# Kernel optimization log

Measured on AMD Instinct MI355X. Metric: run time of the kernel, lower is better.

The kernel has to match this reference:

```python
import jax, jax.numpy as jnp
import numpy as np

P_CLASSES = 1024   # num_classes_per_batch
K_SAMP = 4         # num_samples_per_class
MARGIN = 1.0
EPS = 1e-6
EMBED_DIM = 128


def setup_inputs() -> dict:
    key = jax.random.key(0)
    x = jax.random.normal(key, (P_CLASSES * K_SAMP, EMBED_DIM), dtype=jnp.float32)
    return {"x": x}


def reference(x):
    p, k = P_CLASSES, K_SAMP
    n = p * k
    # pairwise distances D[i,j] = sqrt(relu(|xi|^2 - 2 xi.xj + |xj|^2) + eps)
    norms = jnp.sum(x * x, axis=1)
    D = norms[:, None] - 2.0 * (x @ x.T) + norms[None, :]
    D = jnp.sqrt(jax.nn.relu(D) + EPS)  # [n, n]

    # all positive pairs (i<j) within each class, vectorized over classes
    ii, jj = np.triu_indices(k, 1)                      # [m], m = k*(k-1)/2
    c = np.arange(p)
    ri = (c[:, None] * k + ii[None, :]).reshape(-1)     # [P] = [p*m]
    rj = (c[:, None] * k + jj[None, :]).reshape(-1)
    pair_cls = np.repeat(c, len(ii))                    # class of each pair
    col_cls = np.arange(n) // k                         # class of each column
    neg_mask = jnp.asarray(pair_cls[:, None] != col_cls[None, :])  # [P, n]

    # masked logsumexp over negatives from both anchor rows (concat of the
    # two sliced rows in the original code)
    rows = jnp.concatenate([D[ri], D[rj]], axis=1)                 # [P, 2n]
    mask2 = jnp.concatenate([neg_mask, neg_mask], axis=1)
    vals = jnp.where(mask2, MARGIN - rows, -jnp.inf)
    lse = jax.scipy.special.logsumexp(vals, axis=1)                # [P]

    J = lse + D[ri, rj]
    return jnp.mean(jnp.square(jax.nn.relu(J))) / 2.0
```

## Files before the change

kernel.cpp:

```cpp
#include <hip/hip_runtime.h>

#define NROWS 4096
#define DIM 128
#define PCLS 1024
#define NPAIR 6144
#define MARGIN 1.0f
#define EPS 1e-6f
#define LOG2E 1.4426950408889634f
#define NSPLIT 32

typedef __attribute__((ext_vector_type(8))) short bf16x8;
typedef __attribute__((ext_vector_type(4))) float f32x4;

union FragU { uint4 u; bf16x8 v; };

__device__ __forceinline__ unsigned short f2bf(float f) {
    unsigned int b = __float_as_uint(f);
    b = (b + 0x7FFFu + ((b >> 16) & 1u)) >> 16;
    return (unsigned short)b;
}
__device__ __forceinline__ float bf2f(unsigned short u) {
    return __uint_as_float((unsigned int)u << 16);
}

__global__ void prep_kernel(const float* __restrict__ x,
                            unsigned short* __restrict__ xbf,
                            float* __restrict__ norms) {
    int row = blockIdx.x * 4 + (threadIdx.x >> 6);
    int l = threadIdx.x & 63;
    float2 v = *reinterpret_cast<const float2*>(x + row * DIM + 2 * l);
    unsigned int packed = (unsigned int)f2bf(v.x) | ((unsigned int)f2bf(v.y) << 16);
    *reinterpret_cast<unsigned int*>(xbf + row * DIM + 2 * l) = packed;
    float s = v.x * v.x + v.y * v.y;
    #pragma unroll
    for (int m = 1; m < 64; m <<= 1) s += __shfl_xor(s, m, 64);
    if (l == 0) norms[row] = s;
}

__launch_bounds__(512, 4)
__global__ void main_kernel(const unsigned short* __restrict__ xbf,
                            const float* __restrict__ norms,
                            unsigned short* __restrict__ partial,
                            float* __restrict__ posD) {
    __shared__ __align__(16) unsigned short lds[128 * DIM];
    __shared__ float colW[8 * 128];
    const int t = threadIdx.x;
    const int w = t >> 6;
    const int l = t & 63;
    const int lg = l >> 4;
    const int lr = l & 15;

    int u = blockIdx.x;
    int rb = (int)((65.0f - sqrtf(4225.0f - 8.0f * (float)u)) * 0.5f);
    while (rb > 0 && rb * (65 - rb) / 2 > u) --rb;
    while ((rb + 1) * (64 - rb) / 2 <= u) ++rb;
    const int cb = rb + (u - rb * (65 - rb) / 2);
    const bool offd = (cb != rb);

    const int rbase = rb * 128 + w * 16;
    const int cbase = cb * 128;

    FragU afr[4];
    const char* abase = (const char*)xbf + (size_t)(rbase + lr) * 256 + lg * 16;
    #pragma unroll
    for (int s = 0; s < 4; ++s)
        afr[s].u = *reinterpret_cast<const uint4*>(abase + s * 64);

    float njv[8];
    #pragma unroll
    for (int tile = 0; tile < 8; ++tile)
        njv[tile] = norms[cbase + tile * 16 + lr];

    float ni[4];
    #pragma unroll
    for (int rr = 0; rr < 4; ++rr)
        ni[rr] = norms[rbase + lg * 4 + rr] + EPS;

    #pragma unroll
    for (int it = 0; it < 4; ++it) {
        int lin = it * 8192 + t * 16;
        int col = lin >> 8;
        int inner = lin & 255;
        uint4 v = *reinterpret_cast<const uint4*>(
            (const char*)xbf + (size_t)(cbase + col) * 256 + inner);
        *reinterpret_cast<uint4*>(
            (char*)lds + col * 256 + (inner ^ ((col & 7) << 4))) = v;
    }

    __syncthreads();

    float accS[4] = {0.f, 0.f, 0.f, 0.f};
    float colA[8];

    #pragma unroll
    for (int tile = 0; tile < 8; ++tile) {
        const int lcol = tile * 16 + lr;
        const float nj = njv[tile];
        const char* bbase = (const char*)lds + lcol * 256;
        const int xr = (lcol & 7) << 4;
        f32x4 acc = {0.f, 0.f, 0.f, 0.f};
        #pragma unroll
        for (int s = 0; s < 4; ++s) {
            FragU bu;
            int inner = s * 64 + lg * 16;
            bu.u = *reinterpret_cast<const uint4*>(bbase + (inner ^ xr));
            acc = __builtin_amdgcn_mfma_f32_16x16x32_bf16(afr[s].v, bu.v, acc, 0, 0, 0);
        }
        if (offd) {
            float es = 0.f;
            #pragma unroll
            for (int rr = 0; rr < 4; ++rr) {
                float nn = ni[rr] + nj;
                float d2 = fmaf(-2.0f, acc[rr], nn);
                float d = __builtin_amdgcn_sqrtf(fmaxf(d2, EPS));
                float e = __builtin_amdgcn_exp2f(fmaf(d, -LOG2E, LOG2E));
                accS[rr] += e;
                es += e;
            }
            colA[tile] = es;
        } else if (tile != w) {
            #pragma unroll
            for (int rr = 0; rr < 4; ++rr) {
                float nn = ni[rr] + nj;
                float d2 = fmaf(-2.0f, acc[rr], nn);
                float d = __builtin_amdgcn_sqrtf(fmaxf(d2, EPS));
                accS[rr] += __builtin_amdgcn_exp2f(fmaf(d, -LOG2E, LOG2E));
            }
        } else {
            #pragma unroll
            for (int rr = 0; rr < 4; ++rr) {
                int a = lg * 4 + rr;
                int b = lr;
                float nn = ni[rr] + nj;
                float d2 = fmaf(-2.0f, acc[rr], nn);
                float d = __builtin_amdgcn_sqrtf(fmaxf(d2, EPS));
                float e = __builtin_amdgcn_exp2f(fmaf(d, -LOG2E, LOG2E));
                bool same = (a >> 2) == (b >> 2);
                accS[rr] += same ? 0.f : e;
                if (same && a < b) {
                    int i = a & 3, j = b & 3;
                    int idx = i * (7 - i) / 2 + (j - i - 1);
                    int cls = (rbase + a) >> 2;
                    posD[cls * 6 + idx] = d;
                }
            }
        }
    }

    #pragma unroll
    for (int rr = 0; rr < 4; ++rr) {
        #pragma unroll
        for (int m = 1; m < 16; m <<= 1) accS[rr] += __shfl_xor(accS[rr], m, 64);
    }
    if (lr == 0) {
        #pragma unroll
        for (int rr = 0; rr < 4; ++rr)
            partial[cb * NROWS + rbase + lg * 4 + rr] = f2bf(accS[rr]);
    }

    if (offd) {
        #pragma unroll
        for (int tile = 0; tile < 8; ++tile) {
            colA[tile] += __shfl_xor(colA[tile], 16, 64);
            colA[tile] += __shfl_xor(colA[tile], 32, 64);
        }
        if (l < 16) {
            #pragma unroll
            for (int tile = 0; tile < 8; ++tile)
                colW[w * 128 + tile * 16 + l] = colA[tile];
        }
        __syncthreads();
        if (t < 128) {
            float s = 0.f;
            #pragma unroll
            for (int ww = 0; ww < 8; ++ww) s += colW[ww * 128 + t];
            partial[rb * NROWS + cbase + t] = f2bf(s);
        }
    }
}

__global__ void tail_kernel(const unsigned short* __restrict__ partial,
                            const float* __restrict__ posD,
                            float* __restrict__ out) {
    const int c = threadIdx.x;
    float S[4] = {0.f, 0.f, 0.f, 0.f};
    #pragma unroll
    for (int sp = 0; sp < NSPLIT; ++sp) {
        ushort4 v = *reinterpret_cast<const ushort4*>(partial + sp * NROWS + 4 * c);
        S[0] += bf2f(v.x); S[1] += bf2f(v.y); S[2] += bf2f(v.z); S[3] += bf2f(v.w);
    }
    const int II[6] = {0, 0, 0, 1, 1, 2};
    const int JJ[6] = {1, 2, 3, 2, 3, 3};
    float acc = 0.f;
    #pragma unroll
    for (int p = 0; p < 6; ++p) {
        float d = posD[c * 6 + p];
        float J = __logf(S[II[p]] + S[JJ[p]]) + d;
        float r = fmaxf(J, 0.f);
        acc += r * r;
    }
    #pragma unroll
    for (int m = 1; m < 64; m <<= 1) acc += __shfl_xor(acc, m, 64);
    __shared__ float red[16];
    if ((c & 63) == 0) red[c >> 6] = acc;
    __syncthreads();
    if (c < 64) {
        float v = (c < 16) ? red[c] : 0.f;
        #pragma unroll
        for (int m = 1; m < 16; m <<= 1) v += __shfl_xor(v, m, 64);
        if (c == 0) out[0] = v * (1.0f / (2.0f * (float)NPAIR));
    }
}

extern "C" void kernel_launch(void* const* d_in, const int* in_sizes, int n_in,
                              void* d_out, int out_size, void* d_ws, size_t ws_size,
                              hipStream_t stream) {
    const float* x = (const float*)d_in[0];
    char* ws = (char*)d_ws;
    unsigned short* xbf = (unsigned short*)ws;
    float* norms = (float*)(ws + 1048576);
    unsigned short* partial = (unsigned short*)(ws + 1048576 + 16384);
    float* posD = (float*)(ws + 1048576 + 16384 + 262144);
    float* out = (float*)d_out;

    hipLaunchKernelGGL(prep_kernel, dim3(NROWS / 4), dim3(256), 0, stream, x, xbf, norms);
    hipLaunchKernelGGL(main_kernel, dim3(528), dim3(512), 0, stream, xbf, norms, partial, posD);
    hipLaunchKernelGGL(tail_kernel, dim3(1), dim3(1024), 0, stream, partial, posD, out);
}
```

Before: 25.51 us.

## Fuse bf16 conversion and norm computation into main kernel, drop prep kernel

Removes the separate prep kernel that converted x to bf16 and computed row norms. The main kernel now reads fp32 x directly, computes norms for its 256 rows into shared memory, and converts A fragments and B tiles to bf16 on the fly. This saves a kernel launch and the round trip of the bf16 copy through global memory. In exchange each block recomputes norms and conversions, reads twice as many bytes of fp32 input, and adds more ALU work before the first barrier.

```diff
diff --git a/kernel.cpp b/kernel.cpp
--- a/kernel.cpp
+++ b/kernel.cpp
@@ -12,7 +12,7 @@
 typedef __attribute__((ext_vector_type(8))) short bf16x8;
 typedef __attribute__((ext_vector_type(4))) float f32x4;
 
-union FragU { uint4 u; bf16x8 v; };
+union FragU { uint4 u; bf16x8 v; ushort us[8]; };
 
 __device__ __forceinline__ unsigned short f2bf(float f) {
     unsigned int b = __float_as_uint(f);
@@ -23,27 +23,13 @@
     return __uint_as_float((unsigned int)u << 16);
 }
 
-__global__ void prep_kernel(const float* __restrict__ x,
-                            unsigned short* __restrict__ xbf,
-                            float* __restrict__ norms) {
-    int row = blockIdx.x * 4 + (threadIdx.x >> 6);
-    int l = threadIdx.x & 63;
-    float2 v = *reinterpret_cast<const float2*>(x + row * DIM + 2 * l);
-    unsigned int packed = (unsigned int)f2bf(v.x) | ((unsigned int)f2bf(v.y) << 16);
-    *reinterpret_cast<unsigned int*>(xbf + row * DIM + 2 * l) = packed;
-    float s = v.x * v.x + v.y * v.y;
-    #pragma unroll
-    for (int m = 1; m < 64; m <<= 1) s += __shfl_xor(s, m, 64);
-    if (l == 0) norms[row] = s;
-}
-
 __launch_bounds__(512, 4)
-__global__ void main_kernel(const unsigned short* __restrict__ xbf,
-                            const float* __restrict__ norms,
+__global__ void main_kernel(const float* __restrict__ x,
                             unsigned short* __restrict__ partial,
                             float* __restrict__ posD) {
     __shared__ __align__(16) unsigned short lds[128 * DIM];
     __shared__ float colW[8 * 128];
+    __shared__ float normBuf[256];
     const int t = threadIdx.x;
     const int w = t >> 6;
     const int l = t & 63;
@@ -60,34 +46,56 @@
     const int rbase = rb * 128 + w * 16;
     const int cbase = cb * 128;
 
+    {
+        int idx = t >> 1, half = t & 1;
+        int grow = (idx < 128) ? (rb * 128 + idx) : (cbase + idx - 128);
+        const float4* p = reinterpret_cast<const float4*>(
+            x + (size_t)grow * DIM + half * 64);
+        float s = 0.f;
+        #pragma unroll
+        for (int q = 0; q < 16; ++q) {
+            float4 v = p[q];
+            s = fmaf(v.x, v.x, s); s = fmaf(v.y, v.y, s);
+            s = fmaf(v.z, v.z, s); s = fmaf(v.w, v.w, s);
+        }
+        s += __shfl_xor(s, 1, 64);
+        if (!half) normBuf[idx] = s;
+    }
+
     FragU afr[4];
-    const char* abase = (const char*)xbf + (size_t)(rbase + lr) * 256 + lg * 16;
-    #pragma unroll
-    for (int s = 0; s < 4; ++s)
-        afr[s].u = *reinterpret_cast<const uint4*>(abase + s * 64);
-
-    float njv[8];
-    #pragma unroll
-    for (int tile = 0; tile < 8; ++tile)
-        njv[tile] = norms[cbase + tile * 16 + lr];
-
-    float ni[4];
-    #pragma unroll
-    for (int rr = 0; rr < 4; ++rr)
-        ni[rr] = norms[rbase + lg * 4 + rr] + EPS;
-
-    #pragma unroll
-    for (int it = 0; it < 4; ++it) {
-        int lin = it * 8192 + t * 16;
+    const float* arow = x + (size_t)(rbase + lr) * DIM;
+    #pragma unroll
+    for (int s = 0; s < 4; ++s) {
+        const float4* ap = reinterpret_cast<const float4*>(arow + s * 32 + lg * 8);
+        float4 a0 = ap[0], a1 = ap[1];
+        afr[s].us[0] = f2bf(a0.x); afr[s].us[1] = f2bf(a0.y);
+        afr[s].us[2] = f2bf(a0.z); afr[s].us[3] = f2bf(a0.w);
+        afr[s].us[4] = f2bf(a1.x); afr[s].us[5] = f2bf(a1.y);
+        afr[s].us[6] = f2bf(a1.z); afr[s].us[7] = f2bf(a1.w);
+    }
+
+    #pragma unroll
+    for (int q = 0; q < 8; ++q) {
+        int lin = q * 4096 + t * 8;
         int col = lin >> 8;
         int inner = lin & 255;
-        uint4 v = *reinterpret_cast<const uint4*>(
-            (const char*)xbf + (size_t)(cbase + col) * 256 + inner);
-        *reinterpret_cast<uint4*>(
-            (char*)lds + col * 256 + (inner ^ ((col & 7) << 4))) = v;
+        float4 v = *reinterpret_cast<const float4*>(
+            x + (size_t)(cbase + col) * DIM + (inner >> 1));
+        ushort4 h = { f2bf(v.x), f2bf(v.y), f2bf(v.z), f2bf(v.w) };
+        *reinterpret_cast<ushort4*>(
+            (char*)lds + col * 256 + (inner ^ ((col & 7) << 4))) = h;
     }
 
     __syncthreads();
+
+    float njv[8];
+    #pragma unroll
+    for (int tile = 0; tile < 8; ++tile)
+        njv[tile] = normBuf[128 + tile * 16 + lr];
+    float ni[4];
+    #pragma unroll
+    for (int rr = 0; rr < 4; ++rr)
+        ni[rr] = normBuf[w * 16 + lg * 4 + rr] + EPS;
 
     float accS[4] = {0.f, 0.f, 0.f, 0.f};
     float colA[8];
@@ -217,13 +225,10 @@
                               hipStream_t stream) {
     const float* x = (const float*)d_in[0];
     char* ws = (char*)d_ws;
-    unsigned short* xbf = (unsigned short*)ws;
-    float* norms = (float*)(ws + 1048576);
-    unsigned short* partial = (unsigned short*)(ws + 1048576 + 16384);
-    float* posD = (float*)(ws + 1048576 + 16384 + 262144);
+    unsigned short* partial = (unsigned short*)ws;
+    float* posD = (float*)(ws + 262144);
     float* out = (float*)d_out;
 
-    hipLaunchKernelGGL(prep_kernel, dim3(NROWS / 4), dim3(256), 0, stream, x, xbf, norms);
-    hipLaunchKernelGGL(main_kernel, dim3(528), dim3(512), 0, stream, xbf, norms, partial, posD);
+    hipLaunchKernelGGL(main_kernel, dim3(528), dim3(512), 0, stream, x, partial, posD);
     hipLaunchKernelGGL(tail_kernel, dim3(1), dim3(1024), 0, stream, partial, posD, out);
 }
```

After: 33.01 us. +29.4%, slower.
